# Kernel optimization log

Hardware: AMD Instinct MI355X
Metric: run time of the kernel (lower is better)

## Reference

```python
import jax, jax.numpy as jnp
import numpy as np

V, D, L, H, SLOTS, FF = 32000, 1024, 6, 16, 4096, 4096
DH = D // H

def rmsnorm(x, w, eps=1e-8):
    return x * jax.lax.rsqrt(jnp.mean(x * x, axis=-1, keepdims=True) + eps) * w

def rope(x):
    # x: [B,T,D]; interleaved RoPE over full d_model as in RoPEEmbedding
    T = x.shape[1]
    inv_freq = 1.0 / (10000.0 ** (jnp.arange(0, D, 2, dtype=jnp.float32) / D))
    freqs = jnp.arange(T, dtype=jnp.float32)[:, None] * inv_freq[None, :]  # [T, D/2]
    cos, sin = jnp.cos(freqs), jnp.sin(freqs)
    x1, x2 = x[..., ::2], x[..., 1::2]
    out = jnp.stack([x1 * cos - x2 * sin, x1 * sin + x2 * cos], axis=-1)
    return out.reshape(x.shape)

def block(x, Wq, Wk, Wv, Wo, bo, n1, Wg, Wu, Wd, n2):
    B, T, _ = x.shape
    q = (x @ Wq).reshape(B, T, H, DH)
    k = (x @ Wk).reshape(B, T, H, DH)
    v = (x @ Wv).reshape(B, T, H, DH)
    scores = jnp.einsum('bqhd,bkhd->bhqk', q, k) * (DH ** -0.5)
    attn = jax.nn.softmax(scores, axis=-1)
    o = jnp.einsum('bhqk,bkhd->bqhd', attn, v).reshape(B, T, D)
    x = rmsnorm(x + o @ Wo + bo, n1)
    ff = (jax.nn.silu(x @ Wg) * (x @ Wu)) @ Wd
    return rmsnorm(x + ff, n2)

def setup_inputs() -> dict:
    key = jax.random.key(0)
    ks = jax.random.split(key, 20)
    nrm = lambda k, s: (jax.random.normal(k, s, jnp.float32) * 0.02)
    inp = {
        'ids': jax.random.randint(ks[0], (2, 2048), 0, V),
        'tok_embed': nrm(ks[1], (V, D)),
        'Wq': nrm(ks[2], (L, D, D)), 'Wk': nrm(ks[3], (L, D, D)),
        'Wv': nrm(ks[4], (L, D, D)), 'Wo': nrm(ks[5], (L, D, D)),
        'bo': jnp.zeros((L, D), jnp.float32),
        'n1': jnp.ones((L, D), jnp.float32),
        'Wg': nrm(ks[6], (L, D, FF)), 'Wu': nrm(ks[7], (L, D, FF)),
        'Wd': nrm(ks[8], (L, FF, D)),
        'n2': jnp.ones((L, D), jnp.float32),
        'mem': nrm(ks[9], (SLOTS, D)),
        'Wsp': nrm(ks[10], (D, D)), 'bsp': jnp.zeros((D,), jnp.float32),
        'Wrp': nrm(ks[11], (D, D)), 'brp': jnp.zeros((D,), jnp.float32),
        'nout': jnp.ones((D,), jnp.float32),
    }
    return inp

def reference(ids, tok_embed, Wq, Wk, Wv, Wo, bo, n1, Wg, Wu, Wd, n2,
              mem, Wsp, bsp, Wrp, brp, nout):
    x = tok_embed[ids]            # [B,T,D] gather
    x = rope(x)
    for i in range(L):
        x = block(x, Wq[i], Wk[i], Wv[i], Wo[i], bo[i], n1[i],
                  Wg[i], Wu[i], Wd[i], n2[i])
    # StateBank content-addressed read: route queries over memory slots
    q = x @ Wsp + bsp                                   # [B,T,D]
    slot_scores = jnp.einsum('btd,sd->bts', q, mem) * (D ** -0.5)
    attention_maps = jax.nn.softmax(slot_scores, axis=-1)  # [B,T,SLOTS]
    r = jnp.einsum('bts,sd->btd', attention_maps, mem)     # gather-route read
    r = r @ Wrp + brp
    h = rmsnorm(x + r, nout)
    logits = h @ tok_embed.T      # tied lm_head
    return logits
```

## Files before the change

kernel.cpp:

```cpp
#include <hip/hip_runtime.h>

typedef __bf16 bf16;
typedef __attribute__((ext_vector_type(8))) __bf16 bf16x8;
typedef __attribute__((ext_vector_type(4))) __bf16 bf16x4;
typedef __attribute__((ext_vector_type(4))) float f32x4;

#define NL 6
#define DIM 1024
#define NH 16
#define DH 64
#define TT 2048
#define BB 2
#define BT 4096
#define FFD 4096
#define NSLOT 4096
#define NV 32000

__device__ __forceinline__ void gld16(const void* g, void* l) {
  __builtin_amdgcn_global_load_lds(
      (const __attribute__((address_space(1))) void*)g,
      (__attribute__((address_space(3))) void*)l, 16, 0, 0);
}


__global__ void cvt_bf16(const float* __restrict__ s, bf16* __restrict__ d, long n) {
  long i = ((long)blockIdx.x * 256 + threadIdx.x) * 4;
  if (i + 3 < n) {
    float4 v = *(const float4*)(s + i);
    bf16x4 o = {(bf16)v.x, (bf16)v.y, (bf16)v.z, (bf16)v.w};
    *(bf16x4*)(d + i) = o;
  }
}

__global__ void transpose_cvt(const float* __restrict__ src, bf16* __restrict__ dst, int R, int C) {
  __shared__ float tile[32][33];
  int c0 = blockIdx.x * 32, r0 = blockIdx.y * 32;
  int tx = threadIdx.x, ty = threadIdx.y;
#pragma unroll
  for (int i = 0; i < 4; ++i)
    tile[ty + i * 8][tx] = src[(size_t)(r0 + ty + i * 8) * C + c0 + tx];
  __syncthreads();
#pragma unroll
  for (int i = 0; i < 4; ++i)
    dst[(size_t)(c0 + ty + i * 8) * R + r0 + tx] = (bf16)tile[tx][ty + i * 8];
}

__global__ void transpose_v(const bf16* __restrict__ v, int ldv, bf16* __restrict__ vT) {
  __shared__ bf16 tile[32][33];
  int t0 = blockIdx.x * 32, d0 = blockIdx.y * 32, bh = blockIdx.z;
  int b = bh >> 4, h = bh & 15;
  int tx = threadIdx.x, ty = threadIdx.y;
#pragma unroll
  for (int i = 0; i < 4; ++i)
    tile[ty + i * 8][tx] = v[(size_t)(b * TT + t0 + ty + i * 8) * ldv + h * DH + d0 + tx];
  __syncthreads();
#pragma unroll
  for (int i = 0; i < 4; ++i)
    vT[((size_t)bh * DH + d0 + ty + i * 8) * TT + t0 + tx] = tile[tx][ty + i * 8];
}


__global__ void embed_rope(const int* __restrict__ ids, const float* __restrict__ emb,
                           float* __restrict__ xf, bf16* __restrict__ xb) {
  int bt = blockIdx.x;
  int t = bt & (TT - 1);
  int id = ids[bt];
  const float* row = emb + (size_t)id * DIM;
  for (int p = threadIdx.x; p < DIM / 2; p += 256) {
    float x1 = row[2 * p], x2 = row[2 * p + 1];
    float inv = __expf(-9.210340371976184f * (float)p * (1.0f / 512.0f));
    float ang = (float)t * inv;
    float c = cosf(ang), s = sinf(ang);
    float o1 = x1 * c - x2 * s;
    float o2 = x1 * s + x2 * c;
    size_t base = (size_t)bt * DIM + 2 * p;
    xf[base] = o1; xf[base + 1] = o2;
    xb[base] = (bf16)o1; xb[base + 1] = (bf16)o2;
  }
}

enum { EP_BF16 = 0, EP_F32 = 1, EP_F32_BIAS = 2, EP_BF16_BIAS = 3, EP_SILU_MUL = 4 };


#define GPHASE(KS, MH, LOADB, STG, WAITC)                                         \
  {                                                                               \
    if (LOADB) {                                                                  \
      _Pragma("unroll") for (int j = 0; j < 4; ++j)                               \
          bfr[j] = *(const bf16x8*)&SB[(KS)*8192 + (wn*64 + j*16 + r16)*32 + rchunk]; \
    }                                                                             \
    _Pragma("unroll") for (int i = 0; i < 4; ++i)                                 \
        af[i] = *(const bf16x8*)&SA[(KS)*8192 + (wm*128 + (MH)*64 + i*16 + r16)*32 + rchunk]; \
    STG;                                                                          \
    __builtin_amdgcn_s_barrier();                                                 \
    __builtin_amdgcn_sched_barrier(0);                                            \
    __builtin_amdgcn_s_setprio(1);                                                \
    _Pragma("unroll") for (int i = 0; i < 4; ++i)                                 \
        _Pragma("unroll") for (int j = 0; j < 4; ++j)                             \
            acc[(MH)*4 + i][j] = __builtin_amdgcn_mfma_f32_16x16x32_bf16(         \
                af[i], bfr[j], acc[(MH)*4 + i][j], 0, 0, 0);                      \
    __builtin_amdgcn_s_setprio(0);                                                \
    WAITC;                                                                        \
    __builtin_amdgcn_s_barrier();                                                 \
    __builtin_amdgcn_sched_barrier(0);                                            \
  }

template <int EP>
__global__ __launch_bounds__(512, 1) void gemm8(
    const bf16* __restrict__ A, const bf16* __restrict__ Bt, void* __restrict__ Cp,
    const float* __restrict__ bias, const bf16* __restrict__ aux,
    int M, int N, int K) {
  constexpr int BK = 64;
  __shared__ bf16 Ssh[2 * 2 * 2 * 256 * 32];

  const int tid = threadIdx.x;
  const int lane = tid & 63;
  const int r16 = lane & 15, hi = lane >> 4;
  const int wave = tid >> 6;
  const int wm = wave >> 2, wn = wave & 3;

  const int nwg = gridDim.x;
  const int orig = blockIdx.x;
  const int qq = nwg >> 3, rr = nwg & 7;
  const int xcd = orig & 7, cidx = orig >> 3;
  const int wg = (xcd < rr ? xcd * (qq + 1) : rr * (qq + 1) + (xcd - rr) * qq) + cidx;
  const int gM = M / 256;
  const int m0 = (wg % gM) * 256;
  const int n0 = (wg / gM) * 256;

  const int srow = tid >> 2;
  const int ccol = tid & 3;
  const int skey = (srow >> 1) & 3;
  const int gcol = (ccol ^ skey) * 8;
  const bf16* aS = A + (size_t)(m0 + srow) * K + gcol;
  const bf16* bS = Bt + (size_t)(n0 + srow) * K + gcol;
  const int dst0 = srow * 32 + ccol * 8;

  const int rkey = (r16 >> 1) & 3;
  const int rchunk = (hi ^ rkey) * 8;

  f32x4 acc[8][4] = {};
  const int NT = K / BK;

  {
    bf16* S0A = Ssh;
    bf16* S0B = Ssh + 16384;
    gld16(aS, S0A + dst0);
    gld16(aS + (size_t)128 * K, S0A + 4096 + dst0);
    gld16(bS, S0B + dst0);
    gld16(bS + (size_t)128 * K, S0B + 4096 + dst0);
    gld16(aS + 32, S0A + 8192 + dst0);
    gld16(aS + 32 + (size_t)128 * K, S0A + 8192 + 4096 + dst0);
    gld16(bS + 32, S0B + 8192 + dst0);
    gld16(bS + 32 + (size_t)128 * K, S0B + 8192 + 4096 + dst0);
    asm volatile("s_waitcnt vmcnt(4)" ::: "memory");
    __builtin_amdgcn_s_barrier();
    __builtin_amdgcn_sched_barrier(0);
  }

  for (int t = 0; t < NT; ++t) {
    const int cb = t & 1, nb = cb ^ 1;
    const bool pre = (t + 1) < NT;
    const size_t koff = (size_t)(t + 1) * BK;
    bf16* SA = Ssh + cb * 32768;
    bf16* SB = SA + 16384;
    bf16* NA = Ssh + nb * 32768;
    bf16* NB = NA + 16384;
    bf16x8 af[4], bfr[4];

    GPHASE(0, 0, true,
      { if (pre) { gld16(aS + koff, NA + dst0);
                   gld16(aS + koff + (size_t)128 * K, NA + 4096 + dst0); } },
      {});
    GPHASE(0, 1, false,
      { if (pre) { gld16(bS + koff, NB + dst0);
                   gld16(bS + koff + (size_t)128 * K, NB + 4096 + dst0); } },
      { if (pre) asm volatile("s_waitcnt vmcnt(4)" ::: "memory");
        else     asm volatile("s_waitcnt vmcnt(0)" ::: "memory"); });
    GPHASE(1, 0, true,
      { if (pre) { gld16(aS + koff + 32, NA + 8192 + dst0);
                   gld16(aS + koff + 32 + (size_t)128 * K, NA + 8192 + 4096 + dst0); } },
      {});
    GPHASE(1, 1, false,
      { if (pre) { gld16(bS + koff + 32, NB + 8192 + dst0);
                   gld16(bS + koff + 32 + (size_t)128 * K, NB + 8192 + 4096 + dst0); } },
      { if (pre) asm volatile("s_waitcnt vmcnt(4)" ::: "memory"); });
  }

#pragma unroll
  for (int mi = 0; mi < 8; ++mi) {
    const int m = m0 + wm * 128 + mi * 16 + hi * 4;
#pragma unroll
    for (int j = 0; j < 4; ++j) {
      const int n = n0 + wn * 64 + j * 16 + r16;
#pragma unroll
      for (int q = 0; q < 4; ++q) {
        size_t idx = (size_t)(m + q) * N + n;
        float v = acc[mi][j][q];
        if constexpr (EP == EP_F32) {
          ((float*)Cp)[idx] = v;
        } else if constexpr (EP == EP_F32_BIAS) {
          ((float*)Cp)[idx] = v + bias[n];
        } else if constexpr (EP == EP_BF16) {
          ((bf16*)Cp)[idx] = (bf16)v;
        } else if constexpr (EP == EP_BF16_BIAS) {
          ((bf16*)Cp)[idx] = (bf16)(v + bias[n]);
        } else {
          float sg = v / (1.0f + __expf(-v));
          ((bf16*)Cp)[idx] = (bf16)(sg * (float)aux[idx]);
        }
      }
    }
  }
}


template <int BM, int BN, int WMW, int WNW, int EP>
__global__ __launch_bounds__(WMW * WNW * 64, 2) void gemmk(
    const bf16* __restrict__ A, const bf16* __restrict__ Bt, void* __restrict__ Cp,
    const float* __restrict__ bias, const bf16* __restrict__ aux,
    int M, int N, int K) {
  constexpr int BK = 32;
  constexpr int NWAVE = WMW * WNW;
  constexpr int NTHR = NWAVE * 64;
  constexpr int MF = BM / (WMW * 16);
  constexpr int NF = BN / (WNW * 16);
  constexpr int AE = BM * BK;
  constexpr int BE = BN * BK;
  constexpr int RHALF = NTHR / 4;
  __shared__ bf16 sA[4][AE];
  __shared__ bf16 sB[4][BE];

  const int tid = threadIdx.x;
  const int lane = tid & 63;
  const int r16 = lane & 15, hi = lane >> 4;
  const int wave = tid >> 6;
  const int wm = wave / WNW, wn = wave % WNW;

  const int nwg = gridDim.x;
  const int orig = blockIdx.x;
  const int qq = nwg >> 3, rr = nwg & 7;
  const int xcd = orig & 7, cidx = orig >> 3;
  const int wg = (xcd < rr ? xcd * (qq + 1) : rr * (qq + 1) + (xcd - rr) * qq) + cidx;
  const int gM = M / BM;
  const int m0 = (wg % gM) * BM;
  const int n0 = (wg / gM) * BN;

  const int srow = tid >> 2;
  const int ccol = tid & 3;
  const int skey = (srow >> 1) & 3;
  const int gcol = ((ccol ^ skey)) * 8;
  const bf16* aS = A + (size_t)(m0 + srow) * K + gcol;
  const bf16* bS = Bt + (size_t)(n0 + srow) * K + gcol;
  const int dst0 = srow * BK + ccol * 8;

  const int rkey = (r16 >> 1) & 3;
  const int rchunk = (hi ^ rkey) * 8;

  f32x4 acc[MF][NF] = {};
  const int NT = K / BK;

  gld16(aS, &sA[0][dst0]);
  gld16(aS + (size_t)RHALF * K, &sA[0][dst0 + RHALF * BK]);
  gld16(bS, &sB[0][dst0]);
  gld16(bS + (size_t)RHALF * K, &sB[0][dst0 + RHALF * BK]);
  gld16(aS + BK, &sA[1][dst0]);
  gld16(aS + BK + (size_t)RHALF * K, &sA[1][dst0 + RHALF * BK]);
  gld16(bS + BK, &sB[1][dst0]);
  gld16(bS + BK + (size_t)RHALF * K, &sB[1][dst0 + RHALF * BK]);

  for (int t = 0; t < NT; ++t) {
    const int cb = t & 3;
    const int pb = (t + 2) & 3;
    const bool pre = (t + 2) < NT;
    if (pre) {
      gld16(aS + (size_t)(t + 2) * BK, &sA[pb][dst0]);
      gld16(aS + (size_t)(t + 2) * BK + (size_t)RHALF * K, &sA[pb][dst0 + RHALF * BK]);
    }
    if (pre)             asm volatile("s_waitcnt vmcnt(6)" ::: "memory");
    else if (t + 1 < NT) asm volatile("s_waitcnt vmcnt(4)" ::: "memory");
    else                 asm volatile("s_waitcnt vmcnt(0)" ::: "memory");
    __builtin_amdgcn_s_barrier();
    __builtin_amdgcn_sched_barrier(0);

    bf16x8 bf_[NF];
#pragma unroll
    for (int j = 0; j < NF; ++j)
      bf_[j] = *(const bf16x8*)&sB[cb][(wn * (NF * 16) + j * 16 + r16) * BK + rchunk];
    if (pre) {
      gld16(bS + (size_t)(t + 2) * BK, &sB[pb][dst0]);
      gld16(bS + (size_t)(t + 2) * BK + (size_t)RHALF * K, &sB[pb][dst0 + RHALF * BK]);
    }
    bf16x8 af[MF];
#pragma unroll
    for (int i = 0; i < MF; ++i)
      af[i] = *(const bf16x8*)&sA[cb][(wm * (MF * 16) + i * 16 + r16) * BK + rchunk];
    __builtin_amdgcn_s_setprio(1);
#pragma unroll
    for (int i = 0; i < MF; ++i)
#pragma unroll
      for (int j = 0; j < NF; ++j)
        acc[i][j] = __builtin_amdgcn_mfma_f32_16x16x32_bf16(af[i], bf_[j], acc[i][j], 0, 0, 0);
    __builtin_amdgcn_s_setprio(0);
  }

#pragma unroll
  for (int i = 0; i < MF; ++i) {
    const int m = m0 + wm * (MF * 16) + i * 16 + hi * 4;
#pragma unroll
    for (int j = 0; j < NF; ++j) {
      const int n = n0 + wn * (NF * 16) + j * 16 + r16;
#pragma unroll
      for (int q = 0; q < 4; ++q) {
        size_t idx = (size_t)(m + q) * N + n;
        float v = acc[i][j][q];
        if constexpr (EP == EP_F32) {
          ((float*)Cp)[idx] = v;
        } else if constexpr (EP == EP_F32_BIAS) {
          ((float*)Cp)[idx] = v + bias[n];
        } else if constexpr (EP == EP_BF16) {
          ((bf16*)Cp)[idx] = (bf16)v;
        } else if constexpr (EP == EP_BF16_BIAS) {
          ((bf16*)Cp)[idx] = (bf16)(v + bias[n]);
        } else {
          float sg = v / (1.0f + __expf(-v));
          ((bf16*)Cp)[idx] = (bf16)(sg * (float)aux[idx]);
        }
      }
    }
  }
}


__global__ __launch_bounds__(256, 2) void attn_flash(
    const bf16* __restrict__ Qp, const bf16* __restrict__ Kp, int ldk,
    const bf16* __restrict__ Vt, bf16* __restrict__ Op) {
  __shared__ bf16 Ks[2][128 * 32];
  __shared__ bf16 Vs[4][64 * 32];
  __shared__ bf16 Ps[4][4][16 * 40];
  const int tid = threadIdx.x, lane = tid & 63, wave = tid >> 6;
  const int h = blockIdx.y, b = blockIdx.z;
  const int r16 = lane & 15, hi = lane >> 4;
  const int qrow = blockIdx.x * 64 + wave * 16 + r16;

  bf16x8 qa[2];
  {
    const bf16* qp = Qp + (size_t)(b * TT + qrow) * ldk + h * DH + hi * 8;
    qa[0] = *(const bf16x8*)qp;
    qa[1] = *(const bf16x8*)(qp + 32);
  }
  const bf16* kBase = Kp + (size_t)(b * TT) * ldk + h * DH;
  const bf16* vBase = Vt + (size_t)(b * NH + h) * DH * TT;

  const int srow = tid >> 2, ccol = tid & 3;
  const int skey = (srow >> 1) & 3;
  const int scolS = (ccol ^ skey) * 8;
  const int dstc = ccol * 8;
  const int rkey = (r16 >> 1) & 3;
  const int rchunk = (hi ^ rkey) * 8;

  float m_run[4] = {-1e30f, -1e30f, -1e30f, -1e30f};
  float l_run[4] = {0.f, 0.f, 0.f, 0.f};
  f32x4 oacc[4] = {};

  for (int kt = 0; kt < TT; kt += 128) {
#pragma unroll
    for (int half = 0; half < 2; ++half) {
      gld16(kBase + (size_t)(kt + srow) * ldk + half * 32 + scolS, &Ks[half][srow * 32 + dstc]);
      gld16(kBase + (size_t)(kt + 64 + srow) * ldk + half * 32 + scolS, &Ks[half][(64 + srow) * 32 + dstc]);
    }
#pragma unroll
    for (int ks = 0; ks < 4; ++ks)
      gld16(vBase + (size_t)srow * TT + kt + ks * 32 + scolS, &Vs[ks][srow * 32 + dstc]);
    __syncthreads();

    f32x4 s[8];
#pragma unroll
    for (int kg = 0; kg < 8; ++kg) {
      f32x4 z = {};
      bf16x8 kb0 = *(const bf16x8*)&Ks[0][(kg * 16 + r16) * 32 + rchunk];
      bf16x8 kb1 = *(const bf16x8*)&Ks[1][(kg * 16 + r16) * 32 + rchunk];
      z = __builtin_amdgcn_mfma_f32_16x16x32_bf16(qa[0], kb0, z, 0, 0, 0);
      z = __builtin_amdgcn_mfma_f32_16x16x32_bf16(qa[1], kb1, z, 0, 0, 0);
      s[kg] = z * 0.125f;
    }
#pragma unroll
    for (int i = 0; i < 4; ++i) {
      float pm = s[0][i];
#pragma unroll
      for (int kg = 1; kg < 8; ++kg) pm = fmaxf(pm, s[kg][i]);
      pm = fmaxf(pm, __shfl_xor(pm, 1));
      pm = fmaxf(pm, __shfl_xor(pm, 2));
      pm = fmaxf(pm, __shfl_xor(pm, 4));
      pm = fmaxf(pm, __shfl_xor(pm, 8));
      float mnew = fmaxf(m_run[i], pm);
      float sc = __expf(m_run[i] - mnew);
      m_run[i] = mnew;
      l_run[i] *= sc;
#pragma unroll
      for (int n = 0; n < 4; ++n) oacc[n][i] *= sc;
#pragma unroll
      for (int kg = 0; kg < 8; ++kg) {
        float p = __expf(s[kg][i] - mnew);
        l_run[i] += p;
        Ps[wave][kg >> 1][(hi * 4 + i) * 40 + (kg & 1) * 16 + r16] = (bf16)p;
      }
    }
#pragma unroll
    for (int ks = 0; ks < 4; ++ks) {
      bf16x8 pa = *(const bf16x8*)&Ps[wave][ks][r16 * 40 + hi * 8];
#pragma unroll
      for (int n = 0; n < 4; ++n) {
        bf16x8 vb = *(const bf16x8*)&Vs[ks][(n * 16 + r16) * 32 + rchunk];
        oacc[n] = __builtin_amdgcn_mfma_f32_16x16x32_bf16(pa, vb, oacc[n], 0, 0, 0);
      }
    }
    __syncthreads();
  }

#pragma unroll
  for (int i = 0; i < 4; ++i) {
    float l = l_run[i];
    l += __shfl_xor(l, 1);
    l += __shfl_xor(l, 2);
    l += __shfl_xor(l, 4);
    l += __shfl_xor(l, 8);
    float inv = 1.0f / l;
    int trow = blockIdx.x * 64 + wave * 16 + hi * 4 + i;
    size_t base = ((size_t)b * TT + trow) * DIM + h * DH;
#pragma unroll
    for (int n = 0; n < 4; ++n)
      Op[base + n * 16 + r16] = (bf16)(oacc[n][i] * inv);
  }
}


__global__ __launch_bounds__(256) void resid_rms(
    const float* __restrict__ xin, const float* __restrict__ y, const float* __restrict__ wgt,
    float* __restrict__ xf_out, bf16* __restrict__ xb_out) {
  __shared__ float red[4];
  const int r = blockIdx.x, tid = threadIdx.x;
  const size_t base = (size_t)r * DIM + tid * 4;
  float4 v = *(const float4*)(xin + base);
  float4 u = *(const float4*)(y + base);
  v.x += u.x; v.y += u.y; v.z += u.z; v.w += u.w;
  float ss = v.x * v.x + v.y * v.y + v.z * v.z + v.w * v.w;
#pragma unroll
  for (int d = 1; d < 64; d <<= 1) ss += __shfl_xor(ss, d);
  if ((tid & 63) == 0) red[tid >> 6] = ss;
  __syncthreads();
  ss = red[0] + red[1] + red[2] + red[3];
  float sc = rsqrtf(ss * (1.0f / DIM) + 1e-8f);
  const float4 wv = *(const float4*)(wgt + tid * 4);
  float o0 = v.x * sc * wv.x, o1 = v.y * sc * wv.y, o2 = v.z * sc * wv.z, o3 = v.w * sc * wv.w;
  if (xf_out) {
    float4 ov = {o0, o1, o2, o3};
    *(float4*)(xf_out + base) = ov;
  }
  bf16x4 ob = {(bf16)o0, (bf16)o1, (bf16)o2, (bf16)o3};
  *(bf16x4*)(xb_out + base) = ob;
}


__global__ __launch_bounds__(256) void softmax_rows(const float* __restrict__ Sc, bf16* __restrict__ P) {
  __shared__ float red[4];
  const int r = blockIdx.x, tid = threadIdx.x;
  const float* row = Sc + (size_t)r * NSLOT;
  float4 v[4];
#pragma unroll
  for (int i = 0; i < 4; ++i) v[i] = *(const float4*)(row + tid * 4 + i * 1024);
  float mx = -1e30f;
#pragma unroll
  for (int i = 0; i < 4; ++i)
    mx = fmaxf(fmaxf(fmaxf(fmaxf(mx, v[i].x), v[i].y), v[i].z), v[i].w);
#pragma unroll
  for (int d = 1; d < 64; d <<= 1) mx = fmaxf(mx, __shfl_xor(mx, d));
  if ((tid & 63) == 0) red[tid >> 6] = mx;
  __syncthreads();
  mx = fmaxf(fmaxf(red[0], red[1]), fmaxf(red[2], red[3]));
  __syncthreads();
  float e[16];
  float sum = 0.f;
#pragma unroll
  for (int i = 0; i < 4; ++i) {
    e[i * 4 + 0] = __expf((v[i].x - mx) * 0.03125f);
    e[i * 4 + 1] = __expf((v[i].y - mx) * 0.03125f);
    e[i * 4 + 2] = __expf((v[i].z - mx) * 0.03125f);
    e[i * 4 + 3] = __expf((v[i].w - mx) * 0.03125f);
    sum += e[i * 4 + 0] + e[i * 4 + 1] + e[i * 4 + 2] + e[i * 4 + 3];
  }
#pragma unroll
  for (int d = 1; d < 64; d <<= 1) sum += __shfl_xor(sum, d);
  if ((tid & 63) == 0) red[tid >> 6] = sum;
  __syncthreads();
  sum = red[0] + red[1] + red[2] + red[3];
  float inv = 1.0f / sum;
#pragma unroll
  for (int i = 0; i < 4; ++i) {
    bf16x4 ob = {(bf16)(e[i * 4 + 0] * inv), (bf16)(e[i * 4 + 1] * inv),
                 (bf16)(e[i * 4 + 2] * inv), (bf16)(e[i * 4 + 3] * inv)};
    *(bf16x4*)(P + (size_t)r * NSLOT + tid * 4 + i * 1024) = ob;
  }
}


extern "C" void kernel_launch(void* const* d_in, const int* in_sizes, int n_in,
                              void* d_out, int out_size, void* d_ws, size_t ws_size,
                              hipStream_t stream) {
  (void)in_sizes; (void)n_in; (void)out_size;
  const int* ids = (const int*)d_in[0];
  const float* emb = (const float*)d_in[1];
  const float* Wq = (const float*)d_in[2];
  const float* Wk = (const float*)d_in[3];
  const float* Wv = (const float*)d_in[4];
  const float* Wo = (const float*)d_in[5];
  const float* bo = (const float*)d_in[6];
  const float* n1 = (const float*)d_in[7];
  const float* Wg = (const float*)d_in[8];
  const float* Wu = (const float*)d_in[9];
  const float* Wd = (const float*)d_in[10];
  const float* n2 = (const float*)d_in[11];
  const float* memp = (const float*)d_in[12];
  const float* Wsp = (const float*)d_in[13];
  const float* bsp = (const float*)d_in[14];
  const float* Wrp = (const float*)d_in[15];
  const float* brp = (const float*)d_in[16];
  const float* nout = (const float*)d_in[17];

  char* w = (char*)d_ws;
  auto alloc = [&](size_t bytes) -> void* {
    void* p = (void*)w;
    w += (bytes + 255) & ~(size_t)255;
    return p;
  };

  const size_t dd = (size_t)DIM * DIM;
  const size_t dff = (size_t)DIM * FFD;

  bf16* tok_b = (bf16*)alloc((size_t)NV * DIM * 2);
  bf16* mem_b = (bf16*)alloc((size_t)NSLOT * DIM * 2);
  bf16* memT  = (bf16*)alloc((size_t)NSLOT * DIM * 2);
  bf16* WspT  = (bf16*)alloc(dd * 2);
  bf16* WrpT  = (bf16*)alloc(dd * 2);
  float* xf   = (float*)alloc((size_t)BT * DIM * 4);
  bf16* xb    = (bf16*)alloc((size_t)BT * DIM * 2);
  float* yb   = (float*)alloc((size_t)BT * DIM * 4);
  bf16* W3T   = (bf16*)alloc(3 * dd * 2);
  bf16* WoT   = (bf16*)alloc(dd * 2);
  bf16* WgT   = (bf16*)alloc(dff * 2);
  bf16* WuT   = (bf16*)alloc(dff * 2);
  bf16* WdT   = (bf16*)alloc(dff * 2);
  bf16* qkv   = (bf16*)alloc((size_t)BT * 3 * DIM * 2);
  bf16* vT_   = (bf16*)alloc((size_t)BT * DIM * 2);
  bf16* ot_   = (bf16*)alloc((size_t)BT * DIM * 2);
  bf16* qb    = (bf16*)alloc((size_t)BT * DIM * 2);
  bf16* rb    = (bf16*)alloc((size_t)BT * DIM * 2);
  bf16* hb    = (bf16*)alloc((size_t)BT * DIM * 2);

  size_t used = (size_t)(w - (char*)d_ws);
  size_t region_bytes = (size_t)BT * NSLOT * 4 + (size_t)BT * NSLOT * 2;
  char* region;
  if (used + region_bytes <= ws_size) region = (char*)alloc(region_bytes);
  else region = (char*)d_out;
  bf16* Ub = (bf16*)region;
  bf16* Hb = (bf16*)(region + (size_t)BT * FFD * 2);
  float* scoresF = (float*)region;
  bf16* attnb = (bf16*)(region + (size_t)BT * NSLOT * 4);

  dim3 blkT(32, 8);

  cvt_bf16<<<NV * DIM / 1024, 256, 0, stream>>>(emb, tok_b, (long)NV * DIM);
  cvt_bf16<<<NSLOT * DIM / 1024, 256, 0, stream>>>(memp, mem_b, (long)NSLOT * DIM);
  transpose_cvt<<<dim3(DIM / 32, NSLOT / 32), blkT, 0, stream>>>(memp, memT, NSLOT, DIM);
  transpose_cvt<<<dim3(DIM / 32, DIM / 32), blkT, 0, stream>>>(Wsp, WspT, DIM, DIM);
  transpose_cvt<<<dim3(DIM / 32, DIM / 32), blkT, 0, stream>>>(Wrp, WrpT, DIM, DIM);
  embed_rope<<<BT, 256, 0, stream>>>(ids, emb, xf, xb);

  for (int l = 0; l < NL; ++l) {
    transpose_cvt<<<dim3(32, 32), blkT, 0, stream>>>(Wq + l * dd, W3T, DIM, DIM);
    transpose_cvt<<<dim3(32, 32), blkT, 0, stream>>>(Wk + l * dd, W3T + dd, DIM, DIM);
    transpose_cvt<<<dim3(32, 32), blkT, 0, stream>>>(Wv + l * dd, W3T + 2 * dd, DIM, DIM);
    transpose_cvt<<<dim3(32, 32), blkT, 0, stream>>>(Wo + l * dd, WoT, DIM, DIM);
    transpose_cvt<<<dim3(FFD / 32, DIM / 32), blkT, 0, stream>>>(Wg + l * dff, WgT, DIM, FFD);
    transpose_cvt<<<dim3(FFD / 32, DIM / 32), blkT, 0, stream>>>(Wu + l * dff, WuT, DIM, FFD);
    transpose_cvt<<<dim3(DIM / 32, FFD / 32), blkT, 0, stream>>>(Wd + l * dff, WdT, FFD, DIM);

    gemm8<EP_BF16><<<dim3(16 * 12), 512, 0, stream>>>(
        xb, W3T, qkv, nullptr, nullptr, BT, 3 * DIM, DIM);
    transpose_v<<<dim3(TT / 32, DH / 32, BB * NH), blkT, 0, stream>>>(qkv + 2 * DIM, 3 * DIM, vT_);
    attn_flash<<<dim3(TT / 64, NH, BB), 256, 0, stream>>>(qkv, qkv + DIM, 3 * DIM, vT_, ot_);
    gemmk<128, 128, 2, 2, EP_F32_BIAS><<<dim3(8 * 32), 256, 0, stream>>>(
        ot_, WoT, yb, bo + l * DIM, nullptr, BT, DIM, DIM);
    resid_rms<<<BT, 256, 0, stream>>>(xf, yb, n1 + l * DIM, xf, xb);
    gemm8<EP_BF16><<<dim3(16 * 16), 512, 0, stream>>>(
        xb, WuT, Ub, nullptr, nullptr, BT, FFD, DIM);
    gemm8<EP_SILU_MUL><<<dim3(16 * 16), 512, 0, stream>>>(
        xb, WgT, Hb, nullptr, Ub, BT, FFD, DIM);
    gemmk<128, 128, 2, 2, EP_F32><<<dim3(8 * 32), 256, 0, stream>>>(
        Hb, WdT, yb, nullptr, nullptr, BT, DIM, FFD);
    resid_rms<<<BT, 256, 0, stream>>>(xf, yb, n2 + l * DIM, xf, xb);
  }

  gemmk<128, 128, 2, 2, EP_BF16_BIAS><<<dim3(8 * 32), 256, 0, stream>>>(
      xb, WspT, qb, bsp, nullptr, BT, DIM, DIM);
  gemm8<EP_F32><<<dim3(16 * 16), 512, 0, stream>>>(
      qb, mem_b, scoresF, nullptr, nullptr, BT, NSLOT, DIM);
  softmax_rows<<<BT, 256, 0, stream>>>(scoresF, attnb);
  gemmk<128, 128, 2, 2, EP_BF16><<<dim3(8 * 32), 256, 0, stream>>>(
      attnb, memT, rb, nullptr, nullptr, BT, DIM, NSLOT);
  gemmk<128, 128, 2, 2, EP_F32_BIAS><<<dim3(8 * 32), 256, 0, stream>>>(
      rb, WrpT, yb, brp, nullptr, BT, DIM, DIM);
  resid_rms<<<BT, 256, 0, stream>>>(xf, yb, nout, nullptr, hb);
  gemm8<EP_F32><<<dim3(16 * 125), 512, 0, stream>>>(
      hb, tok_b, (float*)d_out, nullptr, nullptr, BT, NV, DIM);
}
```

Before: 2.918 ms.

## Restructure GEMM mainloop into four-stage BK=32 LDS pipeline with three tiles in flight

```diff
diff --git a/kernel.cpp b/kernel.cpp
--- a/kernel.cpp
+++ b/kernel.cpp
@@ -82,35 +82,12 @@
 enum { EP_BF16 = 0, EP_F32 = 1, EP_F32_BIAS = 2, EP_BF16_BIAS = 3, EP_SILU_MUL = 4 };
 
 
-#define GPHASE(KS, MH, LOADB, STG, WAITC)                                         \
-  {                                                                               \
-    if (LOADB) {                                                                  \
-      _Pragma("unroll") for (int j = 0; j < 4; ++j)                               \
-          bfr[j] = *(const bf16x8*)&SB[(KS)*8192 + (wn*64 + j*16 + r16)*32 + rchunk]; \
-    }                                                                             \
-    _Pragma("unroll") for (int i = 0; i < 4; ++i)                                 \
-        af[i] = *(const bf16x8*)&SA[(KS)*8192 + (wm*128 + (MH)*64 + i*16 + r16)*32 + rchunk]; \
-    STG;                                                                          \
-    __builtin_amdgcn_s_barrier();                                                 \
-    __builtin_amdgcn_sched_barrier(0);                                            \
-    __builtin_amdgcn_s_setprio(1);                                                \
-    _Pragma("unroll") for (int i = 0; i < 4; ++i)                                 \
-        _Pragma("unroll") for (int j = 0; j < 4; ++j)                             \
-            acc[(MH)*4 + i][j] = __builtin_amdgcn_mfma_f32_16x16x32_bf16(         \
-                af[i], bfr[j], acc[(MH)*4 + i][j], 0, 0, 0);                      \
-    __builtin_amdgcn_s_setprio(0);                                                \
-    WAITC;                                                                        \
-    __builtin_amdgcn_s_barrier();                                                 \
-    __builtin_amdgcn_sched_barrier(0);                                            \
-  }
-
 template <int EP>
 __global__ __launch_bounds__(512, 1) void gemm8(
     const bf16* __restrict__ A, const bf16* __restrict__ Bt, void* __restrict__ Cp,
     const float* __restrict__ bias, const bf16* __restrict__ aux,
     int M, int N, int K) {
-  constexpr int BK = 64;
-  __shared__ bf16 Ssh[2 * 2 * 2 * 256 * 32];
+  __shared__ bf16 S[4][2][256 * 32];
 
   const int tid = threadIdx.x;
   const int lane = tid & 63;
@@ -133,57 +110,76 @@
   const int gcol = (ccol ^ skey) * 8;
   const bf16* aS = A + (size_t)(m0 + srow) * K + gcol;
   const bf16* bS = Bt + (size_t)(n0 + srow) * K + gcol;
-  const int dst0 = srow * 32 + ccol * 8;
+  const int dst0 = tid * 8;
 
   const int rkey = (r16 >> 1) & 3;
   const int rchunk = (hi ^ rkey) * 8;
 
   f32x4 acc[8][4] = {};
-  const int NT = K / BK;
-
-  {
-    bf16* S0A = Ssh;
-    bf16* S0B = Ssh + 16384;
-    gld16(aS, S0A + dst0);
-    gld16(aS + (size_t)128 * K, S0A + 4096 + dst0);
-    gld16(bS, S0B + dst0);
-    gld16(bS + (size_t)128 * K, S0B + 4096 + dst0);
-    gld16(aS + 32, S0A + 8192 + dst0);
-    gld16(aS + 32 + (size_t)128 * K, S0A + 8192 + 4096 + dst0);
-    gld16(bS + 32, S0B + 8192 + dst0);
-    gld16(bS + 32 + (size_t)128 * K, S0B + 8192 + 4096 + dst0);
-    asm volatile("s_waitcnt vmcnt(4)" ::: "memory");
+  const int NT = K / 32;
+
+#pragma unroll
+  for (int s = 0; s < 3; ++s) {
+    gld16(aS + s * 32, &S[s][0][dst0]);
+    gld16(aS + s * 32 + (size_t)128 * K, &S[s][0][dst0 + 4096]);
+    gld16(bS + s * 32, &S[s][1][dst0]);
+    gld16(bS + s * 32 + (size_t)128 * K, &S[s][1][dst0 + 4096]);
+  }
+  asm volatile("s_waitcnt vmcnt(8)" ::: "memory");
+  __builtin_amdgcn_s_barrier();
+  __builtin_amdgcn_sched_barrier(0);
+
+  for (int s = 0; s < NT; ++s) {
+    const int cs = s & 3, ps = (s + 3) & 3;
+    const bool pre = (s + 3) < NT;
+    const bf16* SA = S[cs][0];
+    const bf16* SB = S[cs][1];
+    const size_t koff = (size_t)(s + 3) * 32;
+    bf16x8 af[4], bfr[4];
+
+#pragma unroll
+    for (int j = 0; j < 4; ++j)
+      bfr[j] = *(const bf16x8*)&SB[(wn * 64 + j * 16 + r16) * 32 + rchunk];
+#pragma unroll
+    for (int i = 0; i < 4; ++i)
+      af[i] = *(const bf16x8*)&SA[(wm * 128 + i * 16 + r16) * 32 + rchunk];
+    if (pre) {
+      gld16(aS + koff, &S[ps][0][dst0]);
+      gld16(aS + koff + (size_t)128 * K, &S[ps][0][dst0 + 4096]);
+    }
     __builtin_amdgcn_s_barrier();
     __builtin_amdgcn_sched_barrier(0);
-  }
-
-  for (int t = 0; t < NT; ++t) {
-    const int cb = t & 1, nb = cb ^ 1;
-    const bool pre = (t + 1) < NT;
-    const size_t koff = (size_t)(t + 1) * BK;
-    bf16* SA = Ssh + cb * 32768;
-    bf16* SB = SA + 16384;
-    bf16* NA = Ssh + nb * 32768;
-    bf16* NB = NA + 16384;
-    bf16x8 af[4], bfr[4];
-
-    GPHASE(0, 0, true,
-      { if (pre) { gld16(aS + koff, NA + dst0);
-                   gld16(aS + koff + (size_t)128 * K, NA + 4096 + dst0); } },
-      {});
-    GPHASE(0, 1, false,
-      { if (pre) { gld16(bS + koff, NB + dst0);
-                   gld16(bS + koff + (size_t)128 * K, NB + 4096 + dst0); } },
-      { if (pre) asm volatile("s_waitcnt vmcnt(4)" ::: "memory");
-        else     asm volatile("s_waitcnt vmcnt(0)" ::: "memory"); });
-    GPHASE(1, 0, true,
-      { if (pre) { gld16(aS + koff + 32, NA + 8192 + dst0);
-                   gld16(aS + koff + 32 + (size_t)128 * K, NA + 8192 + 4096 + dst0); } },
-      {});
-    GPHASE(1, 1, false,
-      { if (pre) { gld16(bS + koff + 32, NB + 8192 + dst0);
-                   gld16(bS + koff + 32 + (size_t)128 * K, NB + 8192 + 4096 + dst0); } },
-      { if (pre) asm volatile("s_waitcnt vmcnt(4)" ::: "memory"); });
+    __builtin_amdgcn_s_setprio(1);
+#pragma unroll
+    for (int i = 0; i < 4; ++i)
+#pragma unroll
+      for (int j = 0; j < 4; ++j)
+        acc[i][j] = __builtin_amdgcn_mfma_f32_16x16x32_bf16(af[i], bfr[j], acc[i][j], 0, 0, 0);
+    __builtin_amdgcn_s_setprio(0);
+    __builtin_amdgcn_s_barrier();
+    __builtin_amdgcn_sched_barrier(0);
+
+#pragma unroll
+    for (int i = 0; i < 4; ++i)
+      af[i] = *(const bf16x8*)&SA[(wm * 128 + 64 + i * 16 + r16) * 32 + rchunk];
+    if (pre) {
+      gld16(bS + koff, &S[ps][1][dst0]);
+      gld16(bS + koff + (size_t)128 * K, &S[ps][1][dst0 + 4096]);
+    }
+    __builtin_amdgcn_s_barrier();
+    __builtin_amdgcn_sched_barrier(0);
+    __builtin_amdgcn_s_setprio(1);
+#pragma unroll
+    for (int i = 0; i < 4; ++i)
+#pragma unroll
+      for (int j = 0; j < 4; ++j)
+        acc[4 + i][j] = __builtin_amdgcn_mfma_f32_16x16x32_bf16(af[i], bfr[j], acc[4 + i][j], 0, 0, 0);
+    __builtin_amdgcn_s_setprio(0);
+    if (pre)               asm volatile("s_waitcnt vmcnt(8)" ::: "memory");
+    else if ((s + 2) < NT) asm volatile("s_waitcnt vmcnt(4)" ::: "memory");
+    else if ((s + 1) < NT) asm volatile("s_waitcnt vmcnt(0)" ::: "memory");
+    __builtin_amdgcn_s_barrier();
+    __builtin_amdgcn_sched_barrier(0);
   }
 
 #pragma unroll
```

After: 2.924 ms. No clear change (+0.2%).
